# Kernel tuning notes

Hardware: AMD Instinct MI355X
Metric: run time of the kernel (lower is better)

Reference implementation:

```python
import jax, jax.numpy as jnp
import numpy as np

N_NODES = 1024
IN_FEAT = 256
N_HEADS = 4
N_HIDDEN = 32  # out_features, is_concat=False
NEG_SLOPE = 0.2


def setup_inputs() -> dict:
    key = jax.random.key(0)
    k1, k2, k3, k4 = jax.random.split(key, 4)
    h = jax.random.normal(k1, (N_NODES, IN_FEAT), dtype=jnp.float32)
    adj_mat = jax.random.randint(k2, (N_NODES, N_NODES, 1), 0, 2, dtype=jnp.int32)
    W_l = jax.random.normal(k3, (IN_FEAT, N_HEADS * N_HIDDEN), dtype=jnp.float32) * (IN_FEAT ** -0.5)
    attn_w = jax.random.normal(k4, (N_HIDDEN,), dtype=jnp.float32) * (N_HIDDEN ** -0.5)
    return {"h": h, "adj_mat": adj_mat, "W_l": W_l, "attn_w": attn_w}


def reference(h, adj_mat, W_l, attn_w):
    n = h.shape[0]
    # shared weights: g_l == g_r == g, shape [N, H, F]
    g = (h @ W_l).reshape(n, N_HEADS, N_HIDDEN)
    # dense additive scoring: g_sum[i, j] = g_i + g_j  -> [N, N, H, F]
    g_sum = g[:, None, :, :] + g[None, :, :, :]
    # e[i, j, h] = attn(leaky_relu(g_sum))  -> [N, N, H]
    e = jnp.einsum('ijhf,f->ijh', jax.nn.leaky_relu(g_sum, negative_slope=NEG_SLOPE), attn_w)
    # mask non-edges, softmax over source nodes j (dim=1)
    e = jnp.where(adj_mat == 0, -jnp.inf, e)
    a = jax.nn.softmax(e, axis=1)
    # dropout is identity at inference (p applied only in training)
    # weighted aggregation, then mean over heads (is_concat=False)
    attn_res = jnp.einsum('ijh,jhf->ihf', a, g)
    return attn_res.mean(axis=1)
```

## Files before the change

### kernel.cpp

```cpp
#include <hip/hip_runtime.h>
#include <math.h>

#define NN 1024
#define NH 4
#define FH 32
#define FT 128

__global__ __launch_bounds__(256) void gat_gemm(
    const float* __restrict__ h, const float* __restrict__ W,
    const float* __restrict__ attw, float* __restrict__ g,
    float* __restrict__ gT4, float* __restrict__ s06)
{
    const int i0 = blockIdx.x * 4;
    const int t = threadIdx.x;
    __shared__ float hl[4 * 256];
    __shared__ float part[2][4][128];

    reinterpret_cast<float4*>(hl)[t] = reinterpret_cast<const float4*>(h + i0 * 256)[t];
    __syncthreads();

    const int c = t & 127, kh = t >> 7;
    const float* __restrict__ Wp = W + (kh * 128) * FT + c;
    const float* __restrict__ hb = hl + kh * 128;
    float a0 = 0.f, a1 = 0.f, a2 = 0.f, a3 = 0.f;
    #pragma unroll
    for (int k = 0; k < 128; k += 4) {
        const float4 h0 = *reinterpret_cast<const float4*>(hb + 0 * 256 + k);
        const float4 h1 = *reinterpret_cast<const float4*>(hb + 1 * 256 + k);
        const float4 h2 = *reinterpret_cast<const float4*>(hb + 2 * 256 + k);
        const float4 h3 = *reinterpret_cast<const float4*>(hb + 3 * 256 + k);
        const float w0 = Wp[(k + 0) * FT], w1 = Wp[(k + 1) * FT];
        const float w2 = Wp[(k + 2) * FT], w3 = Wp[(k + 3) * FT];
        a0 = fmaf(h0.x, w0, a0); a0 = fmaf(h0.y, w1, a0); a0 = fmaf(h0.z, w2, a0); a0 = fmaf(h0.w, w3, a0);
        a1 = fmaf(h1.x, w0, a1); a1 = fmaf(h1.y, w1, a1); a1 = fmaf(h1.z, w2, a1); a1 = fmaf(h1.w, w3, a1);
        a2 = fmaf(h2.x, w0, a2); a2 = fmaf(h2.y, w1, a2); a2 = fmaf(h2.z, w2, a2); a2 = fmaf(h2.w, w3, a2);
        a3 = fmaf(h3.x, w0, a3); a3 = fmaf(h3.y, w1, a3); a3 = fmaf(h3.z, w2, a3); a3 = fmaf(h3.w, w3, a3);
    }
    part[kh][0][c] = a0; part[kh][1][c] = a1; part[kh][2][c] = a2; part[kh][3][c] = a3;
    __syncthreads();

    if (t < 128) {
        const int hd = t >> 5, f = t & 31;
        const float wf = attw[f];
        #pragma unroll
        for (int n = 0; n < 4; ++n) {
            const float gv = part[0][n][t] + part[1][n][t];
            g[(i0 + n) * FT + t] = gv;
            gT4[((size_t)(hd * 8 + (f >> 2)) * NN + (i0 + n)) * 4 + (f & 3)] = gv;
            float pr = gv * wf;
            #pragma unroll
            for (int d = 1; d < 32; d <<= 1) pr += __shfl_xor(pr, d);
            if (f == 0) s06[hd * NN + i0 + n] = 0.6f * pr;
        }
    }
}

__global__ __launch_bounds__(256, 3) void gat_attn(
    const float* __restrict__ g, const float* __restrict__ gT4,
    const float* __restrict__ s06, const int* __restrict__ adj,
    const float* __restrict__ attw, float* __restrict__ out)
{
    __shared__ int adjl[NN];
    __shared__ alignas(16) float slab[NH][64 * 20];
    __shared__ float red[NH][FH];
    __shared__ float redl[NH];

    const int t = threadIdx.x;
    const int i = blockIdx.x;
    const int hd = __builtin_amdgcn_readfirstlane(t >> 6);
    const int jl = t & 63;

    reinterpret_cast<int4*>(adjl)[t] = reinterpret_cast<const int4*>(adj + (size_t)i * NN)[t];

    float w04[FH], gis[FH];
    #pragma unroll
    for (int u = 0; u < 8; ++u) {
        const float4 wv = *reinterpret_cast<const float4*>(attw + u * 4);
        w04[u * 4 + 0] = 0.4f * wv.x; w04[u * 4 + 1] = 0.4f * wv.y;
        w04[u * 4 + 2] = 0.4f * wv.z; w04[u * 4 + 3] = 0.4f * wv.w;
        const float4 gv = *reinterpret_cast<const float4*>(g + i * FT + hd * FH + u * 4);
        gis[u * 4 + 0] = gv.x; gis[u * 4 + 1] = gv.y;
        gis[u * 4 + 2] = gv.z; gis[u * 4 + 3] = gv.w;
    }
    const float sb = s06[hd * NN + i];
    __syncthreads();

    const float* __restrict__ gtb = gT4 + (size_t)hd * 8 * NN * 4;
    const float* __restrict__ srow = s06 + hd * NN;

    float acc[FH];
    #pragma unroll
    for (int k = 0; k < FH; ++k) acc[k] = 0.f;
    float l = 0.f;

    #pragma unroll 2
    for (int step = 0; step < 16; ++step) {
        const int j = step * 64 + jl;
        float4 q[8];
        #pragma unroll
        for (int u = 0; u < 8; ++u)
            q[u] = *reinterpret_cast<const float4*>(gtb + ((size_t)u * NN + j) * 4);
        const float sjv = srow[j];
        const int am = adjl[j];

        float e0 = 0.f, e1 = 0.f, e2 = 0.f, e3 = 0.f;
        #pragma unroll
        for (int u = 0; u < 8; ++u) {
            e0 = fmaf(w04[4 * u + 0], fabsf(gis[4 * u + 0] + q[u].x), e0);
            e1 = fmaf(w04[4 * u + 1], fabsf(gis[4 * u + 1] + q[u].y), e1);
            e2 = fmaf(w04[4 * u + 2], fabsf(gis[4 * u + 2] + q[u].z), e2);
            e3 = fmaf(w04[4 * u + 3], fabsf(gis[4 * u + 3] + q[u].w), e3);
        }
        const float e = ((e0 + e1) + (e2 + e3)) + (sb + sjv);
        const float p = am ? __expf(e) : 0.f;
        l += p;
        #pragma unroll
        for (int u = 0; u < 8; ++u) {
            acc[4 * u + 0] = fmaf(p, q[u].x, acc[4 * u + 0]);
            acc[4 * u + 1] = fmaf(p, q[u].y, acc[4 * u + 1]);
            acc[4 * u + 2] = fmaf(p, q[u].z, acc[4 * u + 2]);
            acc[4 * u + 3] = fmaf(p, q[u].w, acc[4 * u + 3]);
        }
    }

    #pragma unroll
    for (int d = 1; d < 64; d <<= 1) l += __shfl_xor(l, d);

    float* sl = &slab[hd][jl * 20];
    const int f = jl & 15, grp = jl >> 4;

    *reinterpret_cast<float4*>(sl + 0)  = make_float4(acc[0],  acc[1],  acc[2],  acc[3]);
    *reinterpret_cast<float4*>(sl + 4)  = make_float4(acc[4],  acc[5],  acc[6],  acc[7]);
    *reinterpret_cast<float4*>(sl + 8)  = make_float4(acc[8],  acc[9],  acc[10], acc[11]);
    *reinterpret_cast<float4*>(sl + 12) = make_float4(acc[12], acc[13], acc[14], acc[15]);
    asm volatile("s_waitcnt lgkmcnt(0)" ::: "memory");
    float pa = 0.f;
    #pragma unroll
    for (int r = 0; r < 16; ++r) pa += slab[hd][(grp * 16 + r) * 20 + f];
    pa += __shfl_xor(pa, 16); pa += __shfl_xor(pa, 32);
    asm volatile("s_waitcnt lgkmcnt(0)" ::: "memory");

    *reinterpret_cast<float4*>(sl + 0)  = make_float4(acc[16], acc[17], acc[18], acc[19]);
    *reinterpret_cast<float4*>(sl + 4)  = make_float4(acc[20], acc[21], acc[22], acc[23]);
    *reinterpret_cast<float4*>(sl + 8)  = make_float4(acc[24], acc[25], acc[26], acc[27]);
    *reinterpret_cast<float4*>(sl + 12) = make_float4(acc[28], acc[29], acc[30], acc[31]);
    asm volatile("s_waitcnt lgkmcnt(0)" ::: "memory");
    float pb = 0.f;
    #pragma unroll
    for (int r = 0; r < 16; ++r) pb += slab[hd][(grp * 16 + r) * 20 + f];
    pb += __shfl_xor(pb, 16); pb += __shfl_xor(pb, 32);

    if (jl < 16) { red[hd][jl] = pa; red[hd][16 + jl] = pb; }
    if (jl == 0) redl[hd] = l;
    __syncthreads();

    if (t < FH) {
        float o = 0.f;
        #pragma unroll
        for (int hh = 0; hh < NH; ++hh) o += red[hh][t] / redl[hh];
        out[i * FH + t] = 0.25f * o;
    }
}

extern "C" void kernel_launch(void* const* d_in, const int* in_sizes, int n_in,
                              void* d_out, int out_size, void* d_ws, size_t ws_size,
                              hipStream_t stream) {
    const float* h    = (const float*)d_in[0];
    const int*   adj  = (const int*)d_in[1];
    const float* W    = (const float*)d_in[2];
    const float* attw = (const float*)d_in[3];
    float* out = (float*)d_out;

    float* g   = (float*)d_ws;
    float* gT4 = g + NN * FT;
    float* s06 = gT4 + NN * FT;

    gat_gemm<<<NN / 4, 256, 0, stream>>>(h, W, attw, g, gT4, s06);
    gat_attn<<<NN, 256, 0, stream>>>(g, gT4, s06, adj, attw, out);
}
```

Measured before the change: 90.67 us.

## Process two destination rows per attention block to reuse loaded neighbor features

Each attention block now handles two destination nodes, so every gT4 neighbor tile loaded from memory feeds two score/accumulate computations instead of one. This halves global traffic for the neighbor features and halves the grid size. In exchange, register pressure roughly doubles (two 32-wide accumulators plus two gi vectors), so occupancy is lowered to 2 blocks per SIMD-group, loop unrolling is reduced to 1, and fewer blocks (512) are available to fill the GPU.

Result: faster. 81.80 us (-9.8%).

```diff
diff --git a/kernel.cpp b/kernel.cpp
--- a/kernel.cpp
+++ b/kernel.cpp
@@ -55,45 +55,76 @@
     }
 }
 
-__global__ __launch_bounds__(256, 3) void gat_attn(
+#define REDUCE32(ACC, SL, HD, GRP, F, OUTLO, OUTHI)                                         \
+    {                                                                                       \
+        *reinterpret_cast<float4*>((SL) + 0)  = make_float4(ACC[0],  ACC[1],  ACC[2],  ACC[3]);  \
+        *reinterpret_cast<float4*>((SL) + 4)  = make_float4(ACC[4],  ACC[5],  ACC[6],  ACC[7]);  \
+        *reinterpret_cast<float4*>((SL) + 8)  = make_float4(ACC[8],  ACC[9],  ACC[10], ACC[11]); \
+        *reinterpret_cast<float4*>((SL) + 12) = make_float4(ACC[12], ACC[13], ACC[14], ACC[15]); \
+        asm volatile("s_waitcnt lgkmcnt(0)" ::: "memory");                                  \
+        OUTLO = 0.f;                                                                        \
+        _Pragma("unroll")                                                                   \
+        for (int r = 0; r < 16; ++r) OUTLO += slab[HD][((GRP) * 16 + r) * 20 + (F)];        \
+        OUTLO += __shfl_xor(OUTLO, 16); OUTLO += __shfl_xor(OUTLO, 32);                     \
+        asm volatile("s_waitcnt lgkmcnt(0)" ::: "memory");                                  \
+        *reinterpret_cast<float4*>((SL) + 0)  = make_float4(ACC[16], ACC[17], ACC[18], ACC[19]); \
+        *reinterpret_cast<float4*>((SL) + 4)  = make_float4(ACC[20], ACC[21], ACC[22], ACC[23]); \
+        *reinterpret_cast<float4*>((SL) + 8)  = make_float4(ACC[24], ACC[25], ACC[26], ACC[27]); \
+        *reinterpret_cast<float4*>((SL) + 12) = make_float4(ACC[28], ACC[29], ACC[30], ACC[31]); \
+        asm volatile("s_waitcnt lgkmcnt(0)" ::: "memory");                                  \
+        OUTHI = 0.f;                                                                        \
+        _Pragma("unroll")                                                                   \
+        for (int r = 0; r < 16; ++r) OUTHI += slab[HD][((GRP) * 16 + r) * 20 + (F)];        \
+        OUTHI += __shfl_xor(OUTHI, 16); OUTHI += __shfl_xor(OUTHI, 32);                     \
+        asm volatile("s_waitcnt lgkmcnt(0)" ::: "memory");                                  \
+    }
+
+__global__ __launch_bounds__(256, 2) void gat_attn(
     const float* __restrict__ g, const float* __restrict__ gT4,
     const float* __restrict__ s06, const int* __restrict__ adj,
     const float* __restrict__ attw, float* __restrict__ out)
 {
-    __shared__ int adjl[NN];
+    __shared__ int adjl[2][NN];
     __shared__ alignas(16) float slab[NH][64 * 20];
-    __shared__ float red[NH][FH];
-    __shared__ float redl[NH];
+    __shared__ float red[NH][2][FH];
+    __shared__ float redl[NH][2];
 
     const int t = threadIdx.x;
-    const int i = blockIdx.x;
+    const int i0 = blockIdx.x * 2;
     const int hd = __builtin_amdgcn_readfirstlane(t >> 6);
     const int jl = t & 63;
 
-    reinterpret_cast<int4*>(adjl)[t] = reinterpret_cast<const int4*>(adj + (size_t)i * NN)[t];
-
-    float w04[FH], gis[FH];
+    {
+        const int4* __restrict__ src = reinterpret_cast<const int4*>(adj + (size_t)i0 * NN);
+        int4* dst = reinterpret_cast<int4*>(&adjl[0][0]);
+        dst[t] = src[t];
+        dst[t + 256] = src[t + 256];
+    }
+
+    float w04[FH], gisA[FH], gisB[FH];
     #pragma unroll
     for (int u = 0; u < 8; ++u) {
         const float4 wv = *reinterpret_cast<const float4*>(attw + u * 4);
         w04[u * 4 + 0] = 0.4f * wv.x; w04[u * 4 + 1] = 0.4f * wv.y;
         w04[u * 4 + 2] = 0.4f * wv.z; w04[u * 4 + 3] = 0.4f * wv.w;
-        const float4 gv = *reinterpret_cast<const float4*>(g + i * FT + hd * FH + u * 4);
-        gis[u * 4 + 0] = gv.x; gis[u * 4 + 1] = gv.y;
-        gis[u * 4 + 2] = gv.z; gis[u * 4 + 3] = gv.w;
-    }
-    const float sb = s06[hd * NN + i];
+        const float4 ga = *reinterpret_cast<const float4*>(g + (size_t)i0 * FT + hd * FH + u * 4);
+        gisA[u * 4 + 0] = ga.x; gisA[u * 4 + 1] = ga.y; gisA[u * 4 + 2] = ga.z; gisA[u * 4 + 3] = ga.w;
+        const float4 gb = *reinterpret_cast<const float4*>(g + ((size_t)i0 + 1) * FT + hd * FH + u * 4);
+        gisB[u * 4 + 0] = gb.x; gisB[u * 4 + 1] = gb.y; gisB[u * 4 + 2] = gb.z; gisB[u * 4 + 3] = gb.w;
+    }
+    const float sbA = s06[hd * NN + i0];
+    const float sbB = s06[hd * NN + i0 + 1];
     __syncthreads();
 
     const float* __restrict__ gtb = gT4 + (size_t)hd * 8 * NN * 4;
     const float* __restrict__ srow = s06 + hd * NN;
 
-    float acc[FH];
-    #pragma unroll
-    for (int k = 0; k < FH; ++k) acc[k] = 0.f;
-    float l = 0.f;
-
-    #pragma unroll 2
+    float accA[FH], accB[FH];
+    #pragma unroll
+    for (int k = 0; k < FH; ++k) { accA[k] = 0.f; accB[k] = 0.f; }
+    float lA = 0.f, lB = 0.f;
+
+    #pragma unroll 1
     for (int step = 0; step < 16; ++step) {
         const int j = step * 64 + jl;
         float4 q[8];
@@ -101,64 +132,62 @@
         for (int u = 0; u < 8; ++u)
             q[u] = *reinterpret_cast<const float4*>(gtb + ((size_t)u * NN + j) * 4);
         const float sjv = srow[j];
-        const int am = adjl[j];
-
-        float e0 = 0.f, e1 = 0.f, e2 = 0.f, e3 = 0.f;
+        const int amA = adjl[0][j];
+        const int amB = adjl[1][j];
+
+        float a0 = 0.f, a1 = 0.f, a2 = 0.f, a3 = 0.f;
+        float b0 = 0.f, b1 = 0.f, b2 = 0.f, b3 = 0.f;
         #pragma unroll
         for (int u = 0; u < 8; ++u) {
-            e0 = fmaf(w04[4 * u + 0], fabsf(gis[4 * u + 0] + q[u].x), e0);
-            e1 = fmaf(w04[4 * u + 1], fabsf(gis[4 * u + 1] + q[u].y), e1);
-            e2 = fmaf(w04[4 * u + 2], fabsf(gis[4 * u + 2] + q[u].z), e2);
-            e3 = fmaf(w04[4 * u + 3], fabsf(gis[4 * u + 3] + q[u].w), e3);
+            a0 = fmaf(w04[4 * u + 0], fabsf(gisA[4 * u + 0] + q[u].x), a0);
+            a1 = fmaf(w04[4 * u + 1], fabsf(gisA[4 * u + 1] + q[u].y), a1);
+            a2 = fmaf(w04[4 * u + 2], fabsf(gisA[4 * u + 2] + q[u].z), a2);
+            a3 = fmaf(w04[4 * u + 3], fabsf(gisA[4 * u + 3] + q[u].w), a3);
+            b0 = fmaf(w04[4 * u + 0], fabsf(gisB[4 * u + 0] + q[u].x), b0);
+            b1 = fmaf(w04[4 * u + 1], fabsf(gisB[4 * u + 1] + q[u].y), b1);
+            b2 = fmaf(w04[4 * u + 2], fabsf(gisB[4 * u + 2] + q[u].z), b2);
+            b3 = fmaf(w04[4 * u + 3], fabsf(gisB[4 * u + 3] + q[u].w), b3);
         }
-        const float e = ((e0 + e1) + (e2 + e3)) + (sb + sjv);
-        const float p = am ? __expf(e) : 0.f;
-        l += p;
+        const float eA = ((a0 + a1) + (a2 + a3)) + (sbA + sjv);
+        const float eB = ((b0 + b1) + (b2 + b3)) + (sbB + sjv);
+        const float pA = amA ? __expf(eA) : 0.f;
+        const float pB = amB ? __expf(eB) : 0.f;
+        lA += pA; lB += pB;
         #pragma unroll
         for (int u = 0; u < 8; ++u) {
-            acc[4 * u + 0] = fmaf(p, q[u].x, acc[4 * u + 0]);
-            acc[4 * u + 1] = fmaf(p, q[u].y, acc[4 * u + 1]);
-            acc[4 * u + 2] = fmaf(p, q[u].z, acc[4 * u + 2]);
-            acc[4 * u + 3] = fmaf(p, q[u].w, acc[4 * u + 3]);
+            accA[4 * u + 0] = fmaf(pA, q[u].x, accA[4 * u + 0]);
+            accA[4 * u + 1] = fmaf(pA, q[u].y, accA[4 * u + 1]);
+            accA[4 * u + 2] = fmaf(pA, q[u].z, accA[4 * u + 2]);
+            accA[4 * u + 3] = fmaf(pA, q[u].w, accA[4 * u + 3]);
+            accB[4 * u + 0] = fmaf(pB, q[u].x, accB[4 * u + 0]);
+            accB[4 * u + 1] = fmaf(pB, q[u].y, accB[4 * u + 1]);
+            accB[4 * u + 2] = fmaf(pB, q[u].z, accB[4 * u + 2]);
+            accB[4 * u + 3] = fmaf(pB, q[u].w, accB[4 * u + 3]);
         }
     }
 
     #pragma unroll
-    for (int d = 1; d < 64; d <<= 1) l += __shfl_xor(l, d);
+    for (int d = 1; d < 64; d <<= 1) { lA += __shfl_xor(lA, d); lB += __shfl_xor(lB, d); }
 
     float* sl = &slab[hd][jl * 20];
     const int f = jl & 15, grp = jl >> 4;
-
-    *reinterpret_cast<float4*>(sl + 0)  = make_float4(acc[0],  acc[1],  acc[2],  acc[3]);
-    *reinterpret_cast<float4*>(sl + 4)  = make_float4(acc[4],  acc[5],  acc[6],  acc[7]);
-    *reinterpret_cast<float4*>(sl + 8)  = make_float4(acc[8],  acc[9],  acc[10], acc[11]);
-    *reinterpret_cast<float4*>(sl + 12) = make_float4(acc[12], acc[13], acc[14], acc[15]);
-    asm volatile("s_waitcnt lgkmcnt(0)" ::: "memory");
-    float pa = 0.f;
-    #pragma unroll
-    for (int r = 0; r < 16; ++r) pa += slab[hd][(grp * 16 + r) * 20 + f];
-    pa += __shfl_xor(pa, 16); pa += __shfl_xor(pa, 32);
-    asm volatile("s_waitcnt lgkmcnt(0)" ::: "memory");
-
-    *reinterpret_cast<float4*>(sl + 0)  = make_float4(acc[16], acc[17], acc[18], acc[19]);
-    *reinterpret_cast<float4*>(sl + 4)  = make_float4(acc[20], acc[21], acc[22], acc[23]);
-    *reinterpret_cast<float4*>(sl + 8)  = make_float4(acc[24], acc[25], acc[26], acc[27]);
-    *reinterpret_cast<float4*>(sl + 12) = make_float4(acc[28], acc[29], acc[30], acc[31]);
-    asm volatile("s_waitcnt lgkmcnt(0)" ::: "memory");
-    float pb = 0.f;
-    #pragma unroll
-    for (int r = 0; r < 16; ++r) pb += slab[hd][(grp * 16 + r) * 20 + f];
-    pb += __shfl_xor(pb, 16); pb += __shfl_xor(pb, 32);
-
-    if (jl < 16) { red[hd][jl] = pa; red[hd][16 + jl] = pb; }
-    if (jl == 0) redl[hd] = l;
-    __syncthreads();
-
-    if (t < FH) {
+    float paA, pbA, paB, pbB;
+    REDUCE32(accA, sl, hd, grp, f, paA, pbA);
+    REDUCE32(accB, sl, hd, grp, f, paB, pbB);
+
+    if (jl < 16) {
+        red[hd][0][jl] = paA; red[hd][0][16 + jl] = pbA;
+        red[hd][1][jl] = paB; red[hd][1][16 + jl] = pbB;
+    }
+    if (jl == 0) { redl[hd][0] = lA; redl[hd][1] = lB; }
+    __syncthreads();
+
+    if (t < 64) {
+        const int it = t >> 5, ff = t & 31;
         float o = 0.f;
         #pragma unroll
-        for (int hh = 0; hh < NH; ++hh) o += red[hh][t] / redl[hh];
-        out[i * FH + t] = 0.25f * o;
+        for (int hh = 0; hh < NH; ++hh) o += red[hh][it][ff] / redl[hh][it];
+        out[(i0 + it) * FH + ff] = 0.25f * o;
     }
 }
 
@@ -176,5 +205,5 @@
     float* s06 = gT4 + NN * FT;
 
     gat_gemm<<<NN / 4, 256, 0, stream>>>(h, W, attw, g, gT4, s06);
-    gat_attn<<<NN, 256, 0, stream>>>(g, gT4, s06, adj, attw, out);
+    gat_attn<<<NN / 2, 256, 0, stream>>>(g, gT4, s06, adj, attw, out);
 }
```
